# Performance work log

Measured on AMD Instinct MI355X. Metric: run time of the kernel, lower is better.

## Reference

```python
import jax, jax.numpy as jnp
import numpy as np

D_MODEL = 512
DFF = 2048
TOP_K = 2
EXPERTS_PER_LEVEL = (4, 8)  # hierarchical MoE: 2 levels


def setup_inputs() -> dict:
    key = jax.random.key(0)
    ks = jax.random.split(key, 12)
    def w(k, fan_in, shape):
        return jax.random.normal(k, shape, jnp.float32) * (1.0 / np.sqrt(fan_in))
    def b(k, shape):
        return jax.random.normal(k, shape, jnp.float32) * 0.01
    E0, E1 = EXPERTS_PER_LEVEL
    return {
        "x": jax.random.normal(ks[0], (4, 2048, D_MODEL), jnp.float32),
        # level 0: router + 4 experts (stacked along leading expert axis)
        "Wr0": w(ks[1], D_MODEL, (D_MODEL, E0)),
        "W1_0": w(ks[2], D_MODEL, (E0, D_MODEL, DFF)),
        "b1_0": b(ks[3], (E0, DFF)),
        "W2_0": w(ks[4], DFF, (E0, DFF, D_MODEL)),
        "b2_0": b(ks[5], (E0, D_MODEL)),
        # level 1: router + 8 experts
        "Wr1": w(ks[6], D_MODEL, (D_MODEL, E1)),
        "W1_1": w(ks[7], D_MODEL, (E1, D_MODEL, DFF)),
        "b1_1": b(ks[8], (E1, DFF)),
        "W2_1": w(ks[9], DFF, (E1, DFF, D_MODEL)),
        "b2_1": b(ks[10], (E1, D_MODEL)),
    }


def _moe_level(x, Wr, W1, b1, W2, b2, k):
    # Router: full softmax probs over experts; dispatch = binary top-k mask.
    probs = jax.nn.softmax(jnp.einsum('bsd,de->bse', x, Wr), axis=-1)  # [B,S,E]
    _, top_idx = jax.lax.top_k(probs, k)                               # [B,S,k]
    dispatch = jax.nn.one_hot(top_idx, probs.shape[-1], dtype=x.dtype).sum(axis=-2)  # [B,S,E]
    # Faithful to the source: every expert FFN runs on the MASKED inputs
    # (x * dispatch), then is combined with the FULL router probs.
    xm = x[:, :, None, :] * dispatch[..., None]                        # [B,S,E,D]
    h = jax.nn.relu(jnp.einsum('bsed,edf->bsef', xm, W1) + b1)         # [B,S,E,DFF]
    y = jnp.einsum('bsef,efd->bsed', h, W2) + b2                       # [B,S,E,D]
    return jnp.sum(y * probs[..., None], axis=2)                       # [B,S,D]


def reference(x, Wr0, W1_0, b1_0, W2_0, b2_0, Wr1, W1_1, b1_1, W2_1, b2_1):
    # inference path: dropout is identity, no capacity adaptation
    h0 = _moe_level(x, Wr0, W1_0, b1_0, W2_0, b2_0, TOP_K)
    out = _moe_level(h0, Wr1, W1_1, b1_1, W2_1, b2_1, TOP_K)
    return out
```

## Files before the change

kernel.cpp:

```cpp
#include <hip/hip_runtime.h>
#include <hip/hip_bf16.h>
#include <math.h>

#define TOK   8192
#define DM    512
#define DFFN  2048
#define NE0   4
#define NE1   8

typedef __bf16 bf16;
typedef __bf16 bf16x4 __attribute__((ext_vector_type(4)));
typedef __bf16 bf16x8 __attribute__((ext_vector_type(8)));
typedef float  f32x4  __attribute__((ext_vector_type(4)));

__device__ __forceinline__ double wave_sum_f64(double v){
#pragma unroll
  for (int o = 32; o > 0; o >>= 1) v += __shfl_down(v, o, 64);
  return v;
}
__device__ __forceinline__ float wave_sum_f32(float v){
#pragma unroll
  for (int o = 32; o > 0; o >>= 1) v += __shfl_down(v, o, 64);
  return v;
}

__device__ __forceinline__ void gload16(const bf16* g, bf16* l){
  __builtin_amdgcn_global_load_lds(
      (const __attribute__((address_space(1))) void*)g,
      (__attribute__((address_space(3))) void*)l, 16, 0, 0);
}

__global__ void f32_to_bf16(const float* __restrict__ in, bf16* __restrict__ out, int n){
  int i = blockIdx.x*256 + threadIdx.x;
  if (i < n) out[i] = (bf16)in[i];
}

__global__ void transpose_convert(const float* __restrict__ in, bf16* __restrict__ hi,
                                  bf16* __restrict__ lo, int K, int N){
  __shared__ float tile[64][65];
  int e  = blockIdx.z;
  int n0 = blockIdx.x*64, k0 = blockIdx.y*64;
  const float* src = in + (size_t)e*K*N;
  int c = threadIdx.x & 63, r4 = threadIdx.x >> 6;
#pragma unroll
  for (int i = 0; i < 16; ++i){
    int r = r4*16 + i;
    tile[r][c] = src[(size_t)(k0 + r)*N + n0 + c];
  }
  __syncthreads();
  bf16* dh = hi + (size_t)e*K*N;
  bf16* dl = lo ? (lo + (size_t)e*K*N) : nullptr;
#pragma unroll
  for (int i = 0; i < 16; ++i){
    int r = r4*16 + i;
    float v = tile[c][r];
    size_t o = (size_t)(n0 + r)*K + k0 + c;
    bf16 h = (bf16)v;
    dh[o] = h;
    if (dl) dl[o] = (bf16)(v - (float)h);
  }
}

__global__ void compute_c(const float* __restrict__ W2, const float* __restrict__ b1,
                          const float* __restrict__ b2, float* __restrict__ c){
  int gid = blockIdx.x*256 + threadIdx.x;
  int e = gid >> 9, d = gid & (DM-1);
  int fc = blockIdx.y;
  float acc = (fc == 0) ? b2[gid] : 0.f;
  const float* w  = W2 + (size_t)e*DFFN*DM + (size_t)fc*256*DM + d;
  const float* bb = b1 + e*DFFN + fc*256;
#pragma unroll 4
  for (int f = 0; f < 256; ++f) acc += fmaxf(bb[f], 0.f) * w[(size_t)f*DM];
  atomicAdd(&c[gid], acc);
}

__global__ void compute_M(const float* __restrict__ W2_0, const float* __restrict__ Wr1,
                          float* __restrict__ M, int nrows){
  int wv = threadIdx.x >> 6, lane = threadIdx.x & 63;
  int row = blockIdx.x*4 + wv;
  if (row >= nrows) return;
  const float* w = W2_0 + (size_t)row*DM + lane*8;
  float w8[8];
#pragma unroll
  for (int q = 0; q < 8; ++q) w8[q] = w[q];
  double acc[8] = {0,0,0,0,0,0,0,0};
#pragma unroll
  for (int q = 0; q < 8; ++q){
    const float* wr = Wr1 + (size_t)(lane*8 + q)*NE1;
#pragma unroll
    for (int p = 0; p < 8; ++p) acc[p] += (double)w8[q]*(double)wr[p];
  }
#pragma unroll
  for (int p = 0; p < 8; ++p) acc[p] = wave_sum_f64(acc[p]);
  if (lane == 0){
#pragma unroll
    for (int p = 0; p < 8; ++p) M[(size_t)row*8 + p] = (float)acc[p];
  }
}

__global__ void compute_cb_proj(const float* __restrict__ c0, const float* __restrict__ b2_0,
                                const float* __restrict__ Wr1, double* __restrict__ c0p,
                                double* __restrict__ b2p){
  int t = threadIdx.x;
  if (t >= NE0*NE1) return;
  int e = t >> 3, p = t & 7;
  double a = 0.0, b = 0.0;
  for (int d = 0; d < DM; ++d){
    double w = (double)Wr1[d*NE1 + p];
    a += (double)c0[e*DM + d]  * w;
    b += (double)b2_0[e*DM + d]* w;
  }
  c0p[t] = a; b2p[t] = b;
}

__global__ void prefix_offs(const int* __restrict__ counts, int NE, int* __restrict__ offs){
  if (threadIdx.x == 0){
    int s = 0;
    for (int e = 0; e < NE; ++e){ offs[e] = s; s += counts[e]; }
    offs[NE] = s;
  }
}

__global__ void router0_kernel(const float* __restrict__ x, const float* __restrict__ Wr0,
                               float* __restrict__ probs0, int* __restrict__ idx0,
                               bf16* __restrict__ xhi, bf16* __restrict__ xlo){
  int wv = threadIdx.x >> 6, lane = threadIdx.x & 63;
  int t = blockIdx.x*4 + wv;
  const float* xr = x + (size_t)t*DM + lane*8;
  float xv[8];
#pragma unroll
  for (int i = 0; i < 8; ++i) xv[i] = xr[i];
  bf16x8 hv, lv;
#pragma unroll
  for (int i = 0; i < 8; ++i){
    bf16 h = (bf16)xv[i];
    hv[i] = h;
    lv[i] = (bf16)(xv[i] - (float)h);
  }
  *(bf16x8*)(xhi + (size_t)t*DM + lane*8) = hv;
  *(bf16x8*)(xlo + (size_t)t*DM + lane*8) = lv;

  double lg[NE0];
#pragma unroll
  for (int e = 0; e < NE0; ++e){
    double s = 0.0;
#pragma unroll
    for (int i = 0; i < 8; ++i) s += (double)xv[i] * (double)Wr0[(lane*8 + i)*NE0 + e];
    lg[e] = wave_sum_f64(s);
  }
  if (lane == 0){
    double m = lg[0];
#pragma unroll
    for (int e = 1; e < NE0; ++e) m = fmax(m, lg[e]);
    double den = 0.0, ex[NE0];
#pragma unroll
    for (int e = 0; e < NE0; ++e){ ex[e] = exp(lg[e] - m); den += ex[e]; }
    float pf[NE0];
#pragma unroll
    for (int e = 0; e < NE0; ++e){ pf[e] = (float)(ex[e]/den); probs0[t*NE0 + e] = pf[e]; }
    int e0 = 0;
#pragma unroll
    for (int e = 1; e < NE0; ++e) if (pf[e] > pf[e0]) e0 = e;
    int e1 = (e0 == 0) ? 1 : 0;
#pragma unroll
    for (int e = 0; e < NE0; ++e) if (e != e0 && pf[e] > pf[e1]) e1 = e;
    idx0[t*2 + 0] = e0; idx0[t*2 + 1] = e1;
  }
}

__global__ void router1_kernel(const float* __restrict__ proj, const float* __restrict__ probs0,
                               const int* __restrict__ idx0, const double* __restrict__ c0p,
                               const double* __restrict__ b2p, float* __restrict__ probs1,
                               int* __restrict__ idx1){
  int t = blockIdx.x*256 + threadIdx.x;
  float p0[NE0];
#pragma unroll
  for (int e = 0; e < NE0; ++e) p0[e] = probs0[t*NE0 + e];
  double lg[NE1];
#pragma unroll
  for (int p = 0; p < NE1; ++p){
    double s = 0.0;
#pragma unroll
    for (int e = 0; e < NE0; ++e) s += (double)p0[e] * c0p[e*NE1 + p];
    lg[p] = s;
  }
#pragma unroll
  for (int sl = 0; sl < 2; ++sl){
    int e = idx0[t*2 + sl];
    double pe = (double)p0[e];
    const float* pr = proj + ((size_t)(sl*TOK + t))*NE1;
#pragma unroll
    for (int p = 0; p < NE1; ++p) lg[p] += pe * ((double)pr[p] + b2p[e*NE1 + p] - c0p[e*NE1 + p]);
  }
  double m = lg[0];
#pragma unroll
  for (int p = 1; p < NE1; ++p) m = fmax(m, lg[p]);
  double den = 0.0, ex[NE1];
#pragma unroll
  for (int p = 0; p < NE1; ++p){ ex[p] = exp(lg[p] - m); den += ex[p]; }
  float pf[NE1];
#pragma unroll
  for (int p = 0; p < NE1; ++p){ pf[p] = (float)(ex[p]/den); probs1[t*NE1 + p] = pf[p]; }
  int e0 = 0;
#pragma unroll
  for (int p = 1; p < NE1; ++p) if (pf[p] > pf[e0]) e0 = p;
  int e1 = (e0 == 0) ? 1 : 0;
#pragma unroll
  for (int p = 0; p < NE1; ++p) if (p != e0 && pf[p] > pf[e1]) e1 = p;
  idx1[t*2 + 0] = e0; idx1[t*2 + 1] = e1;
}

__global__ void build_lists(const int* __restrict__ idx, int NE,
                            int* __restrict__ list, int* __restrict__ counts,
                            int* __restrict__ posn){
  __shared__ int lcnt[8];
  __shared__ int lbase[8];
  const int tid = threadIdx.x, lane = tid & 63;
  if (tid < NE) lcnt[tid] = 0;
  __syncthreads();
  const int g = blockIdx.x*1024 + tid;
  const int slot = g >> 13;
  const int t = g & (TOK-1);
  const int e = idx[t*2 + slot];
  int wbase = 0, rank = 0;
  for (int ee = 0; ee < NE; ++ee){
    unsigned long long m = __ballot(e == ee);
    if (e == ee){
      int leader = __builtin_ctzll(m);
      int b = 0;
      if (lane == leader) b = atomicAdd(&lcnt[ee], (int)__popcll(m));
      wbase = __shfl(b, leader, 64);
      rank  = (int)__popcll(m & ((1ull << lane) - 1ull));
    }
  }
  __syncthreads();
  if (tid < NE) lbase[tid] = atomicAdd(&counts[tid], lcnt[tid]);
  __syncthreads();
  const int p = lbase[e] + wbase + rank;
  list[e*TOK + p] = slot*TOK + t;
  posn[slot*TOK + t] = e*16384 + p;
}

__global__ void init_combine(const float* __restrict__ probs, const float* __restrict__ c,
                             int NE, float* __restrict__ tgt){
  int gid = blockIdx.x*256 + threadIdx.x;
  int t = gid >> 9, d = gid & (DM-1);
  float v = 0.f;
  for (int e = 0; e < NE; ++e) v += probs[t*NE + e] * c[e*DM + d];
  tgt[gid] = v;
}

__global__ void gather_combine(const float* __restrict__ init, const float* __restrict__ Y,
                               const int* __restrict__ posn, const int* __restrict__ offs,
                               const float* __restrict__ probs, const float* __restrict__ b2,
                               const float* __restrict__ ce, int NE,
                               float* __restrict__ outF, bf16* __restrict__ outB){
  int gid = blockIdx.x*256 + threadIdx.x;
  int t = gid >> 7, d4 = (gid & 127) << 2;
  f32x4 v = *(const f32x4*)(init + (size_t)t*DM + d4);
#pragma unroll
  for (int sl = 0; sl < 2; ++sl){
    int pv = posn[sl*TOK + t];
    int e = pv >> 14, p = pv & 16383;
    int r = offs[e] + p;
    float g = probs[t*NE + e];
    f32x4 y  = *(const f32x4*)(Y  + (size_t)r*DM + d4);
    f32x4 bb = *(const f32x4*)(b2 + (size_t)e*DM + d4);
    f32x4 cc = *(const f32x4*)(ce + (size_t)e*DM + d4);
#pragma unroll
    for (int q = 0; q < 4; ++q) v[q] += g*(y[q] + bb[q] - cc[q]);
  }
  if (outF) *(f32x4*)(outF + (size_t)t*DM + d4) = v;
  if (outB){
    bf16x4 hb;
#pragma unroll
    for (int q = 0; q < 4; ++q) hb[q] = (bf16)v[q];
    *(bf16x4*)(outB + (size_t)t*DM + d4) = hb;
  }
}

__global__ void proj_from_h(const bf16* __restrict__ Hb, const bf16* __restrict__ Hlo,
                            int FC, int f0, const float* __restrict__ Mproj,
                            const int* __restrict__ list, const int* __restrict__ offs,
                            float* __restrict__ proj){
  int wv = threadIdx.x >> 6, lane = threadIdx.x & 63;
  int rr = blockIdx.x*4 + wv;
  if (rr >= offs[NE0]) return;
  int e = 0;
#pragma unroll
  for (int k = 1; k < NE0; ++k) if (rr >= offs[k]) e = k;
  int r = list[e*TOK + (rr - offs[e])];
  const bf16* hh = Hb  + (size_t)rr*FC;
  const bf16* hl = Hlo + (size_t)rr*FC;
  const float* Me = Mproj + ((size_t)e*DFFN + f0)*8;
  float acc[8] = {0,0,0,0,0,0,0,0};
  for (int c = 0; c < FC; c += 512){
    int fl = c + lane*8;
    if (fl < FC){
      bf16x8 a = *(const bf16x8*)(hh + fl);
      bf16x8 b = *(const bf16x8*)(hl + fl);
#pragma unroll
      for (int q = 0; q < 8; ++q){
        float hv = (float)a[q] + (float)b[q];
        const f32x4* mp = (const f32x4*)(Me + (size_t)(fl + q)*8);
        f32x4 m0 = mp[0], m1 = mp[1];
#pragma unroll
        for (int p = 0; p < 4; ++p){
          acc[p]   += hv * m0[p];
          acc[4+p] += hv * m1[p];
        }
      }
    }
  }
#pragma unroll
  for (int p = 0; p < 8; ++p) acc[p] = wave_sum_f32(acc[p]);
  if (lane == 0){
#pragma unroll
    for (int p = 0; p < 8; ++p) proj[(size_t)r*8 + p] += acc[p];
  }
}


template<int SPLIT>
__global__ __launch_bounds__(256, 2) void gemm_ffn1(
    const bf16* __restrict__ Ahi, const bf16* __restrict__ Alo,
    const bf16* __restrict__ Bhi, const bf16* __restrict__ Blo,
    const float* __restrict__ b1,
    const int* __restrict__ list, const int* __restrict__ counts,
    const int* __restrict__ offs,
    bf16* __restrict__ Hb, bf16* __restrict__ Hlo, int f0, int FC)
{
  constexpr int BUFE  = SPLIT ? 16384 : 8192;
  constexpr int SMEME = (2*BUFE > 17408) ? 2*BUFE : 17408;
  __shared__ alignas(16) bf16 smem[SMEME];

  const int e   = blockIdx.z;
  const int cnt = counts[e];
  const int bx = blockIdx.x, by = blockIdx.y;
  int xl, yl;
  if (gridDim.y == 16){
    xl = ((by >> 1) << 3) + (bx >> 3);
    yl = ((bx & 7) << 1) + (by & 1);
  } else { xl = bx; yl = by; }
  const int m0 = xl * 128;
  if (m0 >= cnt) return;
  const int rbase = offs[e] + m0;
  const int n0  = yl * 128;
  const int ng0 = f0 + n0;

  const int tid  = threadIdx.x;
  const int lane = tid & 63, wv = tid >> 6;
  const int wm = wv >> 1, wn = wv & 1;
  const int quad = lane >> 4, l15 = lane & 15;
  const int* le = list + e*TOK;

  const int strow = tid >> 2;
  const int ch8   = (((tid & 3) ^ ((tid >> 3) & 3)) << 3);
  int growR[2];
#pragma unroll
  for (int p = 0; p < 2; ++p){
    int m = m0 + p*64 + strow;
    growR[p] = (m < cnt) ? (le[m] & (TOK-1)) : 0;
  }
  const bf16* Bh = Bhi + (size_t)e*DFFN*DM;
  const bf16* Bl = SPLIT ? (Blo + (size_t)e*DFFN*DM) : nullptr;

  f32x4 acc[4][4];
#pragma unroll
  for (int i = 0; i < 4; ++i)
#pragma unroll
    for (int j = 0; j < 4; ++j) acc[i][j] = (f32x4){0.f,0.f,0.f,0.f};

  const int swzl = (l15 >> 1) & 3;
  int aPos[4], bPos[4];
#pragma unroll
  for (int i = 0; i < 4; ++i){
    aPos[i] = (wm*256 + (i*16 + l15)*4 + (quad ^ swzl)) * 8;
    bPos[i] = (wn*256 + (i*16 + l15)*4 + (quad ^ swzl)) * 8;
  }

  auto stage = [&](int ks, int buf){
    const int colo = (ks << 5) + ch8;
    bf16* dst = smem + buf*BUFE;
#pragma unroll
    for (int p = 0; p < 2; ++p){
      gload16(Ahi + (size_t)growR[p]*DM + colo,                  dst +         (p*256 + tid)*8);
      gload16(Bh  + (size_t)(ng0 + p*64 + strow)*DM + colo,      dst + 4096  + (p*256 + tid)*8);
      if (SPLIT){
        gload16(Alo + (size_t)growR[p]*DM + colo,                dst + 8192  + (p*256 + tid)*8);
        gload16(Bl  + (size_t)(ng0 + p*64 + strow)*DM + colo,    dst + 12288 + (p*256 + tid)*8);
      }
    }
  };

  constexpr int NIT = DM/32;
  stage(0, 0);
  stage(1, 1);
  int cur = 0;
  for (int ks = 0; ks < NIT; ++ks){
    if (ks + 1 < NIT){
      if (SPLIT) asm volatile("s_waitcnt vmcnt(8)" ::: "memory");
      else       asm volatile("s_waitcnt vmcnt(4)" ::: "memory");
    } else {
      asm volatile("s_waitcnt vmcnt(0)" ::: "memory");
    }
    __builtin_amdgcn_sched_barrier(0);
    __builtin_amdgcn_s_barrier();
    __builtin_amdgcn_sched_barrier(0);
    const bf16* B0 = smem + cur*BUFE;
    bf16x8 ah[4], bh[4];
#pragma unroll
    for (int i = 0; i < 4; ++i){
      ah[i] = *(const bf16x8*)&B0[aPos[i]];
      bh[i] = *(const bf16x8*)&B0[4096 + bPos[i]];
    }
#pragma unroll
    for (int i = 0; i < 4; ++i)
#pragma unroll
      for (int j = 0; j < 4; ++j)
        acc[i][j] = __builtin_amdgcn_mfma_f32_16x16x32_bf16(ah[i], bh[j], acc[i][j], 0,0,0);
    if (SPLIT){
      bf16x8 t2[4];
#pragma unroll
      for (int i = 0; i < 4; ++i) t2[i] = *(const bf16x8*)&B0[12288 + bPos[i]];
#pragma unroll
      for (int i = 0; i < 4; ++i)
#pragma unroll
        for (int j = 0; j < 4; ++j)
          acc[i][j] = __builtin_amdgcn_mfma_f32_16x16x32_bf16(ah[i], t2[j], acc[i][j], 0,0,0);
#pragma unroll
      for (int i = 0; i < 4; ++i) t2[i] = *(const bf16x8*)&B0[8192 + aPos[i]];
#pragma unroll
      for (int i = 0; i < 4; ++i)
#pragma unroll
        for (int j = 0; j < 4; ++j)
          acc[i][j] = __builtin_amdgcn_mfma_f32_16x16x32_bf16(t2[i], bh[j], acc[i][j], 0,0,0);
    }
    asm volatile("s_waitcnt lgkmcnt(0)" ::: "memory");
    __builtin_amdgcn_sched_barrier(0);
    __builtin_amdgcn_s_barrier();
    __builtin_amdgcn_sched_barrier(0);
    if (ks + 2 < NIT) stage(ks + 2, cur);
    cur ^= 1;
  }

  float bjv[4];
#pragma unroll
  for (int j = 0; j < 4; ++j)
    bjv[j] = b1[e*DFFN + ng0 + wn*64 + j*16 + l15];

  bf16* Cs = smem;
#pragma unroll
  for (int i = 0; i < 4; ++i)
#pragma unroll
    for (int j = 0; j < 4; ++j)
#pragma unroll
      for (int reg = 0; reg < 4; ++reg){
        float h = fmaxf(acc[i][j][reg] + bjv[j], 0.f);
        Cs[(wm*64 + i*16 + quad*4 + reg)*136 + wn*64 + j*16 + l15] = (bf16)h;
      }
  __syncthreads();
  {
    const int srow = tid >> 1, shalf = (tid & 1) * 64;
    if (m0 + srow < cnt){
      bf16* dst = Hb + (size_t)(rbase + srow)*FC + n0 + shalf;
      const bf16* srcl = &Cs[srow*136 + shalf];
#pragma unroll
      for (int q = 0; q < 8; ++q)
        *(bf16x8*)(dst + q*8) = *(const bf16x8*)(srcl + q*8);
    }
  }
  if (SPLIT){
    __syncthreads();
#pragma unroll
    for (int i = 0; i < 4; ++i)
#pragma unroll
      for (int j = 0; j < 4; ++j)
#pragma unroll
        for (int reg = 0; reg < 4; ++reg){
          float h = fmaxf(acc[i][j][reg] + bjv[j], 0.f);
          bf16 hi = (bf16)h;
          Cs[(wm*64 + i*16 + quad*4 + reg)*136 + wn*64 + j*16 + l15] = (bf16)(h - (float)hi);
        }
    __syncthreads();
    const int srow = tid >> 1, shalf = (tid & 1) * 64;
    if (m0 + srow < cnt){
      bf16* dst = Hlo + (size_t)(rbase + srow)*FC + n0 + shalf;
      const bf16* srcl = &Cs[srow*136 + shalf];
#pragma unroll
      for (int q = 0; q < 8; ++q)
        *(bf16x8*)(dst + q*8) = *(const bf16x8*)(srcl + q*8);
    }
  }
}

__global__ __launch_bounds__(256, 3) void gemm_ffn2(
    const bf16* __restrict__ Hb, int FC, int f0,
    const bf16* __restrict__ Bt,
    const float* __restrict__ b2, const float* __restrict__ ce,
    const float* __restrict__ probs, int NE,
    const int* __restrict__ list, const int* __restrict__ counts,
    const int* __restrict__ offs,
    float* __restrict__ tgt, int addBias, float* __restrict__ Y)
{
  __shared__ alignas(16) bf16 smem[16384];

  const int e   = blockIdx.z;
  const int cnt = counts[e];
  const int bx = blockIdx.x, by = blockIdx.y;
  const int xl = (bx >> 3) + (((bx & 1) + (by << 1)) << 3);
  const int yl = (bx & 7) >> 1;
  const int m0 = xl*128;
  if (m0 >= cnt) return;
  const int rbase = offs[e];
  const int n0  = yl*128;

  const int tid = threadIdx.x, lane = tid & 63, wv = tid >> 6;
  const int wm = wv >> 1, wn = wv & 1, quad = lane >> 4, l15 = lane & 15;
  const int* le = list + e*TOK;

  const int strow = tid >> 2;
  const int ch8   = (((tid & 3) ^ ((tid >> 3) & 3)) << 3);
  int growR[2];
#pragma unroll
  for (int p = 0; p < 2; ++p){
    int m = m0 + p*64 + strow;
    growR[p] = rbase + ((m < cnt) ? m : (cnt - 1));
  }
  const bf16* Be = Bt + (size_t)e*DM*DFFN;

  f32x4 acc[4][4];
#pragma unroll
  for (int i = 0; i < 4; ++i)
#pragma unroll
    for (int j = 0; j < 4; ++j) acc[i][j] = (f32x4){0.f,0.f,0.f,0.f};

  const int swzl = (l15 >> 1) & 3;
  int aPos[4], bPos[4];
#pragma unroll
  for (int i = 0; i < 4; ++i){
    aPos[i] = (wm*256 + (i*16 + l15)*4 + (quad ^ swzl)) * 8;
    bPos[i] = (wn*256 + (i*16 + l15)*4 + (quad ^ swzl)) * 8;
  }

  auto stage = [&](int ks, int buf){
    const int colo = (ks << 5) + ch8;
    bf16* dst = smem + buf*8192;
#pragma unroll
    for (int p = 0; p < 2; ++p){
      gload16(Hb + (size_t)growR[p]*FC + colo,                       dst +        (p*256 + tid)*8);
      gload16(Be + (size_t)(n0 + p*64 + strow)*DFFN + f0 + colo,     dst + 4096 + (p*256 + tid)*8);
    }
  };

  const int NIT = FC/32;
  stage(0, 0);
  stage(1, 1);
  int cur = 0;
  for (int ks = 0; ks < NIT; ++ks){
    if (ks + 1 < NIT) asm volatile("s_waitcnt vmcnt(4)" ::: "memory");
    else              asm volatile("s_waitcnt vmcnt(0)" ::: "memory");
    __builtin_amdgcn_sched_barrier(0);
    __builtin_amdgcn_s_barrier();
    __builtin_amdgcn_sched_barrier(0);
    const bf16* B0 = smem + cur*8192;
    bf16x8 a[4], b[4];
#pragma unroll
    for (int i = 0; i < 4; ++i){
      a[i] = *(const bf16x8*)&B0[aPos[i]];
      b[i] = *(const bf16x8*)&B0[4096 + bPos[i]];
    }
#pragma unroll
    for (int i = 0; i < 4; ++i)
#pragma unroll
      for (int j = 0; j < 4; ++j)
        acc[i][j] = __builtin_amdgcn_mfma_f32_16x16x32_bf16(a[i], b[j], acc[i][j], 0,0,0);
    asm volatile("s_waitcnt lgkmcnt(0)" ::: "memory");
    __builtin_amdgcn_sched_barrier(0);
    __builtin_amdgcn_s_barrier();
    __builtin_amdgcn_sched_barrier(0);
    if (ks + 2 < NIT) stage(ks + 2, cur);
    cur ^= 1;
  }
  if (Y){
#pragma unroll
    for (int i = 0; i < 4; ++i){
#pragma unroll
      for (int reg = 0; reg < 4; ++reg){
        int m = m0 + wm*64 + i*16 + quad*4 + reg;
        if (m >= cnt) continue;
        float* yr = Y + (size_t)(rbase + m)*DM + n0;
#pragma unroll
        for (int j = 0; j < 4; ++j)
          yr[wn*64 + j*16 + l15] = acc[i][j][reg];
      }
    }
  } else {
#pragma unroll
    for (int i = 0; i < 4; ++i){
#pragma unroll
      for (int reg = 0; reg < 4; ++reg){
        int m = m0 + wm*64 + i*16 + quad*4 + reg;
        if (m >= cnt) continue;
        int r = le[m];
        int t = r & (TOK-1);
        float g = probs[t*NE + e];
#pragma unroll
        for (int j = 0; j < 4; ++j){
          int n = n0 + wn*64 + j*16 + l15;
          float v = acc[i][j][reg];
          if (addBias) v += b2[e*DM + n] - ce[e*DM + n];
          atomicAdd(&tgt[(size_t)t*DM + n], g*v);
        }
      }
    }
  }
}

extern "C" void kernel_launch(void* const* d_in, const int* in_sizes, int n_in,
                              void* d_out, int out_size, void* d_ws, size_t ws_size,
                              hipStream_t stream)
{
  (void)in_sizes; (void)n_in; (void)out_size;
  const float* x    = (const float*)d_in[0];
  const float* Wr0  = (const float*)d_in[1];
  const float* W1_0 = (const float*)d_in[2];
  const float* b1_0 = (const float*)d_in[3];
  const float* W2_0 = (const float*)d_in[4];
  const float* b2_0 = (const float*)d_in[5];
  const float* Wr1  = (const float*)d_in[6];
  const float* W1_1 = (const float*)d_in[7];
  const float* b1_1 = (const float*)d_in[8];
  const float* W2_1 = (const float*)d_in[9];
  const float* b2_1 = (const float*)d_in[10];
  float* out = (float*)d_out;

  const size_t MB = (size_t)1 << 20;
  char* base = (char*)d_ws;

  bf16* xhi  = (bf16*)base;
  bf16* h0b  = (bf16*)base;
  bf16* xlo  = (bf16*)(base + 8*MB);
  bf16* w10h = (bf16*)(base + 16*MB);
  bf16* w10l = (bf16*)(base + 32*MB);
  bf16* w11h = (bf16*)(base + 16*MB);
  bf16* w21h = (bf16*)(base + 32*MB);
  bf16* w20h = (bf16*)(base + 48*MB);
  float* h0f = (float*)(base + 64*MB);

  char* mp = base + 80*MB;
  auto take = [&](size_t n) -> char* { char* p = mp; mp += (n + 255) & ~(size_t)255; return p; };
  float* probs0 = (float*)take((size_t)TOK*NE0*4);
  float* probs1 = (float*)take((size_t)TOK*NE1*4);
  int*   idx0   = (int*)  take((size_t)TOK*2*4);
  int*   idx1   = (int*)  take((size_t)TOK*2*4);
  int*   posn0  = (int*)  take((size_t)TOK*2*4);
  int*   posn1  = (int*)  take((size_t)TOK*2*4);
  int*   list0  = (int*)  take((size_t)NE0*TOK*4);
  int*   list1  = (int*)  take((size_t)NE1*TOK*4);
  int*   counts = (int*)  take(256);
  int*   offs0  = (int*)  take(256);
  int*   offs1  = (int*)  take(256);
  float* c0     = (float*)take((size_t)NE0*DM*4);
  float* c1     = (float*)take((size_t)NE1*DM*4);
  float* Mproj  = (float*)take((size_t)NE0*DFFN*NE1*4);
  double* c0p   = (double*)take(NE0*NE1*8);
  double* b2p   = (double*)take(NE0*NE1*8);
  float* proj   = (float*)take((size_t)2*TOK*NE1*4);

  const size_t fixed = 84*MB;
  int NCH;
  if      (ws_size >= fixed + 128*MB) NCH = 1;
  else if (ws_size >= fixed +  64*MB) NCH = 2;
  else if (ws_size >= fixed +  32*MB) NCH = 4;
  else if (ws_size >= fixed +  16*MB) NCH = 8;
  else return;
  const int FC = DFFN / NCH;
  const size_t chunkB = (size_t)2*TOK*FC*2;
  bf16* Hb   = (bf16*)(base + fixed);
  bf16* Hlo  = (bf16*)(base + fixed + chunkB);
  const bool useY = (NCH == 1);
  float* Ybuf = (float*)Hlo;

  hipMemsetAsync(counts, 0, 16*sizeof(int), stream);
  hipMemsetAsync(c0, 0, (size_t)(NE0+NE1)*DM*4, stream);
  hipMemsetAsync(proj, 0, (size_t)2*TOK*NE1*4, stream);

  transpose_convert<<<dim3(DFFN/64, DM/64, NE0), 256, 0, stream>>>(W1_0, w10h, w10l, DM, DFFN);
  transpose_convert<<<dim3(DM/64, DFFN/64, NE0), 256, 0, stream>>>(W2_0, w20h, nullptr, DFFN, DM);
  compute_c<<<dim3(NE0*DM/256, 8), 256, 0, stream>>>(W2_0, b1_0, b2_0, c0);
  compute_c<<<dim3(NE1*DM/256, 8), 256, 0, stream>>>(W2_1, b1_1, b2_1, c1);
  compute_M<<<dim3(NE0*DFFN/4), 256, 0, stream>>>(W2_0, Wr1, Mproj, NE0*DFFN);
  compute_cb_proj<<<1, 64, 0, stream>>>(c0, b2_0, Wr1, c0p, b2p);

  router0_kernel<<<dim3(TOK/4), 256, 0, stream>>>(x, Wr0, probs0, idx0, xhi, xlo);
  build_lists<<<dim3(2*TOK/1024), 1024, 0, stream>>>(idx0, NE0, list0, counts, posn0);
  prefix_offs<<<1, 64, 0, stream>>>(counts, NE0, offs0);
  init_combine<<<dim3(TOK*DM/256), 256, 0, stream>>>(probs0, c0, NE0, h0f);
  for (int c = 0; c < NCH; ++c){
    gemm_ffn1<1><<<dim3(64, FC/128, NE0), 256, 0, stream>>>(
        xhi, xlo, w10h, w10l, b1_0, list0, counts, offs0, Hb, Hlo, c*FC, FC);
    proj_from_h<<<dim3(2*TOK/4), 256, 0, stream>>>(Hb, Hlo, FC, c*FC, Mproj,
                                                   list0, offs0, proj);
    gemm_ffn2<<<dim3(64, DM/128, NE0), 256, 0, stream>>>(
        Hb, FC, c*FC, w20h, b2_0, c0, probs0, NE0, list0, counts, offs0, h0f, (c == 0),
        useY ? Ybuf : nullptr);
  }

  transpose_convert<<<dim3(DFFN/64, DM/64, NE1), 256, 0, stream>>>(W1_1, w11h, nullptr, DM, DFFN);
  transpose_convert<<<dim3(DM/64, DFFN/64, NE1), 256, 0, stream>>>(W2_1, w21h, nullptr, DFFN, DM);
  if (useY){
    gather_combine<<<dim3(TOK*DM/4/256), 256, 0, stream>>>(
        h0f, Ybuf, posn0, offs0, probs0, b2_0, c0, NE0, nullptr, h0b);
  } else {
    f32_to_bf16<<<dim3(TOK*DM/256), 256, 0, stream>>>(h0f, h0b, TOK*DM);
  }
  router1_kernel<<<dim3(TOK/256), 256, 0, stream>>>(proj, probs0, idx0, c0p, b2p,
                                                    probs1, idx1);
  build_lists<<<dim3(2*TOK/1024), 1024, 0, stream>>>(idx1, NE1, list1, counts + NE0, posn1);
  prefix_offs<<<1, 64, 0, stream>>>(counts + NE0, NE1, offs1);
  init_combine<<<dim3(TOK*DM/256), 256, 0, stream>>>(probs1, c1, NE1, out);

  for (int c = 0; c < NCH; ++c){
    gemm_ffn1<0><<<dim3(64, FC/128, NE1), 256, 0, stream>>>(
        h0b, nullptr, w11h, nullptr, b1_1, list1, counts + NE0, offs1,
        Hb, nullptr, c*FC, FC);
    gemm_ffn2<<<dim3(64, DM/128, NE1), 256, 0, stream>>>(
        Hb, FC, c*FC, w21h, b2_1, c1, probs1, NE1, list1, counts + NE0, offs1, out, (c == 0),
        useY ? Ybuf : nullptr);
  }
  if (useY){
    gather_combine<<<dim3(TOK*DM/4/256), 256, 0, stream>>>(
        out, Ybuf, posn1, offs1, probs1, b2_1, c1, NE1, out, nullptr);
  }
}
```

Measured before the change: 807.9 us.

## Split FFN2 K dimension in two halves and fold init_combine into gather

When the single-chunk Y path is used, gemm_ffn2 launches twice as many blocks, each covering half the DFF reduction, and writes partial results to two separate Y buffers. gather_combine sums both partials and computes the probs-weighted c term itself, so the separate init_combine launches are skipped. compute_c is also split into 32 chunks along F instead of 8, giving more parallelism. This adds occupancy for the expert GEMM at the cost of twice the Y traffic and a larger workspace footprint for the second Y buffer.

Result: faster. 732.4 us (-9.3%).

```diff
diff --git a/kernel.cpp b/kernel.cpp
--- a/kernel.cpp
+++ b/kernel.cpp
@@ -67,10 +67,10 @@
   int e = gid >> 9, d = gid & (DM-1);
   int fc = blockIdx.y;
   float acc = (fc == 0) ? b2[gid] : 0.f;
-  const float* w  = W2 + (size_t)e*DFFN*DM + (size_t)fc*256*DM + d;
-  const float* bb = b1 + e*DFFN + fc*256;
+  const float* w  = W2 + (size_t)e*DFFN*DM + (size_t)fc*64*DM + d;
+  const float* bb = b1 + e*DFFN + fc*64;
 #pragma unroll 4
-  for (int f = 0; f < 256; ++f) acc += fmaxf(bb[f], 0.f) * w[(size_t)f*DM];
+  for (int f = 0; f < 64; ++f) acc += fmaxf(bb[f], 0.f) * w[(size_t)f*DM];
   atomicAdd(&c[gid], acc);
 }
 
@@ -250,25 +250,33 @@
   tgt[gid] = v;
 }
 
-__global__ void gather_combine(const float* __restrict__ init, const float* __restrict__ Y,
+__global__ void gather_combine(const float* __restrict__ Y,
                                const int* __restrict__ posn, const int* __restrict__ offs,
                                const float* __restrict__ probs, const float* __restrict__ b2,
                                const float* __restrict__ ce, int NE,
                                float* __restrict__ outF, bf16* __restrict__ outB){
   int gid = blockIdx.x*256 + threadIdx.x;
   int t = gid >> 7, d4 = (gid & 127) << 2;
-  f32x4 v = *(const f32x4*)(init + (size_t)t*DM + d4);
+  const float* Y2 = Y + (size_t)16384*DM;
+  f32x4 v = (f32x4){0.f,0.f,0.f,0.f};
+  for (int e = 0; e < NE; ++e){
+    float pe = probs[t*NE + e];
+    f32x4 cc = *(const f32x4*)(ce + (size_t)e*DM + d4);
+#pragma unroll
+    for (int q = 0; q < 4; ++q) v[q] += pe*cc[q];
+  }
 #pragma unroll
   for (int sl = 0; sl < 2; ++sl){
     int pv = posn[sl*TOK + t];
     int e = pv >> 14, p = pv & 16383;
     int r = offs[e] + p;
     float g = probs[t*NE + e];
-    f32x4 y  = *(const f32x4*)(Y  + (size_t)r*DM + d4);
+    f32x4 y1 = *(const f32x4*)(Y  + (size_t)r*DM + d4);
+    f32x4 y2 = *(const f32x4*)(Y2 + (size_t)r*DM + d4);
     f32x4 bb = *(const f32x4*)(b2 + (size_t)e*DM + d4);
     f32x4 cc = *(const f32x4*)(ce + (size_t)e*DM + d4);
 #pragma unroll
-    for (int q = 0; q < 4; ++q) v[q] += g*(y[q] + bb[q] - cc[q]);
+    for (int q = 0; q < 4; ++q) v[q] += g*(y1[q] + y2[q] + bb[q] - cc[q]);
   }
   if (outF) *(f32x4*)(outF + (size_t)t*DM + d4) = v;
   if (outB){
@@ -508,12 +516,16 @@
   const int e   = blockIdx.z;
   const int cnt = counts[e];
   const int bx = blockIdx.x, by = blockIdx.y;
-  const int xl = (bx >> 3) + (((bx & 1) + (by << 1)) << 3);
+  const int byn = Y ? (by & 3) : by;
+  const int kh  = Y ? (by >> 2) : 0;
+  const int xl = (bx >> 3) + (((bx & 1) + (byn << 1)) << 3);
   const int yl = (bx & 7) >> 1;
   const int m0 = xl*128;
   if (m0 >= cnt) return;
   const int rbase = offs[e];
   const int n0  = yl*128;
+  const int FCk  = Y ? (FC >> 1) : FC;
+  const int kOff = kh * FCk;
 
   const int tid = threadIdx.x, lane = tid & 63, wv = tid >> 6;
   const int wm = wv >> 1, wn = wv & 1, quad = lane >> 4, l15 = lane & 15;
@@ -544,7 +556,7 @@
   }
 
   auto stage = [&](int ks, int buf){
-    const int colo = (ks << 5) + ch8;
+    const int colo = kOff + (ks << 5) + ch8;
     bf16* dst = smem + buf*8192;
 #pragma unroll
     for (int p = 0; p < 2; ++p){
@@ -553,7 +565,7 @@
     }
   };
 
-  const int NIT = FC/32;
+  const int NIT = FCk/32;
   stage(0, 0);
   stage(1, 1);
   int cur = 0;
@@ -583,13 +595,14 @@
     cur ^= 1;
   }
   if (Y){
+    float* Yb = Y + (size_t)kh*16384*DM;
 #pragma unroll
     for (int i = 0; i < 4; ++i){
 #pragma unroll
       for (int reg = 0; reg < 4; ++reg){
         int m = m0 + wm*64 + i*16 + quad*4 + reg;
         if (m >= cnt) continue;
-        float* yr = Y + (size_t)(rbase + m)*DM + n0;
+        float* yr = Yb + (size_t)(rbase + m)*DM + n0;
 #pragma unroll
         for (int j = 0; j < 4; ++j)
           yr[wn*64 + j*16 + l15] = acc[i][j][reg];
@@ -688,21 +701,21 @@
 
   transpose_convert<<<dim3(DFFN/64, DM/64, NE0), 256, 0, stream>>>(W1_0, w10h, w10l, DM, DFFN);
   transpose_convert<<<dim3(DM/64, DFFN/64, NE0), 256, 0, stream>>>(W2_0, w20h, nullptr, DFFN, DM);
-  compute_c<<<dim3(NE0*DM/256, 8), 256, 0, stream>>>(W2_0, b1_0, b2_0, c0);
-  compute_c<<<dim3(NE1*DM/256, 8), 256, 0, stream>>>(W2_1, b1_1, b2_1, c1);
+  compute_c<<<dim3(NE0*DM/256, 32), 256, 0, stream>>>(W2_0, b1_0, b2_0, c0);
+  compute_c<<<dim3(NE1*DM/256, 32), 256, 0, stream>>>(W2_1, b1_1, b2_1, c1);
   compute_M<<<dim3(NE0*DFFN/4), 256, 0, stream>>>(W2_0, Wr1, Mproj, NE0*DFFN);
   compute_cb_proj<<<1, 64, 0, stream>>>(c0, b2_0, Wr1, c0p, b2p);
 
   router0_kernel<<<dim3(TOK/4), 256, 0, stream>>>(x, Wr0, probs0, idx0, xhi, xlo);
   build_lists<<<dim3(2*TOK/1024), 1024, 0, stream>>>(idx0, NE0, list0, counts, posn0);
   prefix_offs<<<1, 64, 0, stream>>>(counts, NE0, offs0);
-  init_combine<<<dim3(TOK*DM/256), 256, 0, stream>>>(probs0, c0, NE0, h0f);
+  if (!useY) init_combine<<<dim3(TOK*DM/256), 256, 0, stream>>>(probs0, c0, NE0, h0f);
   for (int c = 0; c < NCH; ++c){
     gemm_ffn1<1><<<dim3(64, FC/128, NE0), 256, 0, stream>>>(
         xhi, xlo, w10h, w10l, b1_0, list0, counts, offs0, Hb, Hlo, c*FC, FC);
     proj_from_h<<<dim3(2*TOK/4), 256, 0, stream>>>(Hb, Hlo, FC, c*FC, Mproj,
                                                    list0, offs0, proj);
-    gemm_ffn2<<<dim3(64, DM/128, NE0), 256, 0, stream>>>(
+    gemm_ffn2<<<dim3(64, useY ? 8 : 4, NE0), 256, 0, stream>>>(
         Hb, FC, c*FC, w20h, b2_0, c0, probs0, NE0, list0, counts, offs0, h0f, (c == 0),
         useY ? Ybuf : nullptr);
   }
@@ -711,7 +724,7 @@
   transpose_convert<<<dim3(DM/64, DFFN/64, NE1), 256, 0, stream>>>(W2_1, w21h, nullptr, DFFN, DM);
   if (useY){
     gather_combine<<<dim3(TOK*DM/4/256), 256, 0, stream>>>(
-        h0f, Ybuf, posn0, offs0, probs0, b2_0, c0, NE0, nullptr, h0b);
+        Ybuf, posn0, offs0, probs0, b2_0, c0, NE0, nullptr, h0b);
   } else {
     f32_to_bf16<<<dim3(TOK*DM/256), 256, 0, stream>>>(h0f, h0b, TOK*DM);
   }
@@ -719,18 +732,18 @@
                                                     probs1, idx1);
   build_lists<<<dim3(2*TOK/1024), 1024, 0, stream>>>(idx1, NE1, list1, counts + NE0, posn1);
   prefix_offs<<<1, 64, 0, stream>>>(counts + NE0, NE1, offs1);
-  init_combine<<<dim3(TOK*DM/256), 256, 0, stream>>>(probs1, c1, NE1, out);
+  if (!useY) init_combine<<<dim3(TOK*DM/256), 256, 0, stream>>>(probs1, c1, NE1, out);
 
   for (int c = 0; c < NCH; ++c){
     gemm_ffn1<0><<<dim3(64, FC/128, NE1), 256, 0, stream>>>(
         h0b, nullptr, w11h, nullptr, b1_1, list1, counts + NE0, offs1,
         Hb, nullptr, c*FC, FC);
-    gemm_ffn2<<<dim3(64, DM/128, NE1), 256, 0, stream>>>(
+    gemm_ffn2<<<dim3(64, useY ? 8 : 4, NE1), 256, 0, stream>>>(
         Hb, FC, c*FC, w21h, b2_1, c1, probs1, NE1, list1, counts + NE0, offs1, out, (c == 0),
         useY ? Ybuf : nullptr);
   }
   if (useY){
     gather_combine<<<dim3(TOK*DM/4/256), 256, 0, stream>>>(
-        out, Ybuf, posn1, offs1, probs1, b2_1, c1, NE1, out, nullptr);
-  }
-}
+        Ybuf, posn1, offs1, probs1, b2_1, c1, NE1, out, nullptr);
+  }
+}
```
